# Performance work log

Hardware: AMD Instinct MI355X
Metric: run time of the kernel (lower is better)

The kernel has to match this reference:

```python
import jax, jax.numpy as jnp
from jax import lax
import numpy as np

K = 4            # prototypes per class: 3 kmeans centroids + 1 backbone
EPS = 0.1        # sinkhorn entropic regularization
MAX_ITER = 100
THRESH = 0.01
KM_ITERS = 10    # Lloyd iterations (replaces host-side sklearn KMeans)
HW = 28          # the original reshapes pred to 28x28, fixing n = 784


def setup_inputs():
    key = jax.random.key(0)
    k1, k2, k3, k4 = jax.random.split(key, 4)
    b, n, d, c = 32, HW * HW, 1024, 20
    return {
        "query": jax.random.normal(k1, (b, n, d), dtype=jnp.float32),
        "score": jax.random.uniform(k2, (b, n, c), dtype=jnp.float32),
        "label": jax.random.randint(k3, (b, c), 0, 2),
        "gt": jax.random.randint(k4, (b, HW, HW), 0, c + 1),
        "weights": jnp.array([1.0, 1.0, 0.0, -1.0], dtype=jnp.float32),
    }


def _assign(dq, cen, selfm):
    # dq [b,m,d], cen [b,c,j,d], selfm [b,c,m] float mask -> one-hot labels, counts
    x2 = jnp.sum(dq * dq, axis=-1)                                   # [b,m]
    d2 = (x2[:, None, :, None]
          - 2.0 * jnp.einsum('bmd,bcjd->bcmj', dq, cen)
          + jnp.sum(cen * cen, axis=-1)[:, :, None, :])              # [b,c,m,j]
    oh = jax.nn.one_hot(jnp.argmin(d2, axis=-1), cen.shape[2], dtype=dq.dtype) * selfm[..., None]
    return oh, oh.sum(axis=2)


def _sinkhorn(Km, u, v):
    # vectorized over the [b,c] pair grid, per-pair early exit as in the torch loop
    def cond(st):
        it, r, cc, done = st
        return (it < MAX_ITER) & jnp.logical_not(jnp.all(done))

    def body(st):
        it, r, cc, done = st
        r1 = u / jnp.einsum('bcnj,bcj->bcn', Km, cc)
        c1 = v / jnp.einsum('bcnj,bcn->bcj', Km, r1)
        err = jnp.mean(jnp.abs(r1 - r), axis=-1)                     # [b,c]
        r = jnp.where(done[..., None], r, r1)
        cc = jnp.where(done[..., None], cc, c1)
        done = done | (err < THRESH)
        return it + 1, r, cc, done

    st = (jnp.int32(0), jnp.ones_like(u), jnp.ones_like(v),
          jnp.zeros(Km.shape[:2], dtype=bool))
    _, r, cc, _ = lax.while_loop(cond, body, st)
    return r[..., :, None] * cc[..., None, :] * Km                   # [b,c,n,K]


def _forward(query, score, label, gt, weights):
    b, n, d = query.shape
    c = score.shape[2]
    dq, ds = query[:, ::2, :], score[:, ::2, :]                      # stride-2 downsample
    m = dq.shape[1]
    cls_assign = jnp.argmax(ds, axis=-1)                             # [b,m]
    sel = cls_assign[:, None, :] == jnp.arange(c)[None, :, None]     # [b,c,m]
    selfm = sel.astype(query.dtype)
    cnt = selfm.sum(-1)                                              # [b,c]
    valid = (label > 0) & (cnt >= K)

    # ---- masked Lloyd's k-means with k-1 = 3 clusters per (image, class) pair
    order = jnp.argsort((~sel).astype(jnp.int32), axis=-1)           # masked points first
    init_idx = order[..., :K - 1]                                    # [b,c,3]
    cen = dq[jnp.arange(b)[:, None, None], init_idx]                 # [b,c,3,d]

    def km_step(cen, _):
        oh, kcnt = _assign(dq, cen, selfm)
        sums = jnp.einsum('bmd,bcmj->bcjd', dq, oh)
        cen = jnp.where(kcnt[..., None] > 0,
                        sums / jnp.maximum(kcnt, 1.0)[..., None], cen)
        return cen, None

    cen, _ = lax.scan(km_step, cen, None, length=KM_ITERS)
    oh, kcnt = _assign(dq, cen, selfm)                               # final labels

    # ---- sort centroids by mean cluster score (descending)
    sm = ds.mean(axis=-1)                                            # [b,m]
    avg = jnp.where(kcnt > 0,
                    jnp.einsum('bm,bcmj->bcj', sm, oh) / jnp.maximum(kcnt, 1.0),
                    -jnp.inf)
    ordj = jnp.argsort(-avg, axis=-1)                                # [b,c,3]
    cen = jnp.take_along_axis(cen, ordj[..., None], axis=2)

    # ---- backbone prototype = mean over unselected downsampled tokens
    un = 1.0 - selfm
    backbone = jnp.einsum('bmd,bcm->bcd', dq, un) / jnp.maximum(m - cnt, 1.0)[..., None]
    protos = jnp.concatenate([cen, backbone[:, :, None, :]], axis=2)  # [b,c,4,d]

    # ---- OT between query[0] tokens and the 4 prototypes (original uses query[0] always)
    q0 = query[0]
    q0h = q0 / jnp.maximum(jnp.linalg.norm(q0, axis=-1, keepdims=True), 1e-12)
    ph = protos / jnp.maximum(jnp.linalg.norm(protos, axis=-1, keepdims=True), 1e-12)
    sim = jnp.einsum('nd,bcjd->bcnj', q0h, ph)                       # [b,c,n,4]
    Km = lax.stop_gradient(jnp.exp(-(1.0 - sim) / EPS))              # torch.no_grad
    u = jnp.full((b, c, n), 1.0 / n, dtype=query.dtype)
    v = jnp.full((b, c, K), 1.0 / K, dtype=query.dtype)
    T = lax.stop_gradient(_sinkhorn(Km, u, v))                       # [b,c,n,4]

    valid = valid & jnp.logical_not(jnp.any(jnp.isnan(T), axis=(2, 3)))
    pred = jnp.einsum('bcnj,j->bcn', T, weights)                     # [b,c,n]

    # ---- BCE vs gt masks (28x28 -> 28x28 bilinear resize is the identity)
    y = (gt.reshape(b, -1)[:, None, :] == (jnp.arange(c) + 1)[None, :, None]).astype(pred.dtype)
    p = jnp.clip(pred, 0.0, 1.0)
    bce = -(y * jnp.maximum(jnp.log(p), -100.0)
            + (1.0 - y) * jnp.maximum(jnp.log(1.0 - p), -100.0)).mean(axis=-1)  # [b,c]
    bce = jnp.where(valid, bce, 0.0)
    total_n = valid.sum().astype(pred.dtype)
    return bce.sum() / (total_n + 1e-4)


def reference(query, score, label, gt, weights):
    return _forward(query, score, label, gt, weights)
```

## Files before the change

### kernel.cpp

```cpp
#include <hip/hip_runtime.h>
#include <cmath>

#define BB 32
#define NN 784
#define MM 392
#define DD 1024
#define CC 20
#define JJ 3
#define KP 4
#define KM_ITERS 10
#define GMAX 64
#define SKK 3

__global__ void k_cls(const float* __restrict__ score, int* __restrict__ cls,
                      float* __restrict__ sm, int* __restrict__ cnt) {
  int t = blockIdx.x * blockDim.x + threadIdx.x;
  if (t >= BB * MM) return;
  int b = t / MM, i = t - b * MM;
  const float* s = score + ((size_t)b * NN + 2 * i) * CC;
  float best = s[0]; int bi = 0; float acc = s[0];
  #pragma unroll
  for (int c = 1; c < CC; c++) { float v = s[c]; acc += v; if (v > best) { best = v; bi = c; } }
  cls[t] = bi;
  sm[t] = acc / (float)CC;
  atomicAdd(&cnt[b * CC + bi], 1);
}

__global__ void k_valid(const int* __restrict__ label, const int* __restrict__ cnt,
                        int* __restrict__ vlist, int* __restrict__ cpos, int* __restrict__ nvp) {
  __shared__ int sf[1024];
  int t = threadIdx.x;
  int flag = 0;
  if (t < BB * CC) flag = (label[t] > 0 && cnt[t] >= KP) ? 1 : 0;
  sf[t] = flag;
  __syncthreads();
  for (int off = 1; off < 1024; off <<= 1) {
    int v = sf[t];
    int add = (t >= off) ? sf[t - off] : 0;
    __syncthreads();
    sf[t] = v + add;
    __syncthreads();
  }
  if (t < BB * CC) {
    int pos = sf[t] - flag;
    cpos[t] = flag ? pos : -1;
    if (flag) vlist[pos] = t;
  }
  if (t == 0) *nvp = sf[BB * CC - 1];
}

__global__ __launch_bounds__(512) void k_gram(
    const float* __restrict__ query, const int* __restrict__ cls,
    const int* __restrict__ cpos, const float* __restrict__ sm,
    int* __restrict__ glist, int* __restrict__ gmcnt,
    float* __restrict__ classsum, float* __restrict__ wsort) {
  int bc = blockIdx.x; int b = bc / CC, c = bc - b * CC;
  int tid = threadIdx.x, lane = tid & 63, wv = tid >> 6;
  const float* qb = query + (size_t)b * NN * DD;
  __shared__ int s_scan[512];
  __shared__ int s_list[GMAX];
  __shared__ __align__(16) float Xs[GMAX][68];
  __shared__ float Gl[GMAX][65];
  __shared__ float s_w[JJ][GMAX];

  int flag = 0;
  if (tid < MM) flag = (cls[b * MM + tid] == c) ? 1 : 0;
  s_scan[tid] = flag;
  __syncthreads();
  for (int off = 1; off < 512; off <<= 1) {
    int v = s_scan[tid];
    int add = (tid >= off) ? s_scan[tid - off] : 0;
    __syncthreads();
    s_scan[tid] = v + add;
    __syncthreads();
  }
  if (tid < MM && flag) { int pp = s_scan[tid] - 1; if (pp < GMAX) s_list[pp] = tid; }
  __syncthreads();
  int mc = s_scan[MM - 1]; if (mc > GMAX) mc = GMAX;
  if (tid < mc) glist[bc * GMAX + tid] = s_list[tid];
  if (tid == 0) gmcnt[bc] = mc;
  bool valid = (cpos[bc] >= 0);

  int npairs = mc * (mc + 1) / 2;
  int pi[5], pj[5];
  float pacc[5];
  #pragma unroll
  for (int s = 0; s < 5; s++) {
    pacc[s] = 0.f; pi[s] = -1; pj[s] = 0;
    int p = tid + s * 512;
    if (valid && p < npairs) {
      int i = (int)floorf((sqrtf(8.0f * (float)p + 1.0f) - 1.0f) * 0.5f);
      while ((i + 1) * (i + 2) / 2 <= p) i++;
      while (i * (i + 1) / 2 > p) i--;
      pi[s] = i; pj[s] = p - i * (i + 1) / 2;
    }
  }

  for (int ch = 0; ch < DD / 64; ch++) {
    __syncthreads();
    for (int e = tid; e < mc * 16; e += 512) {
      int row = e >> 4, c4 = e & 15;
      float4 v = *(const float4*)(qb + (size_t)(2 * s_list[row]) * DD + ch * 64 + c4 * 4);
      *(float4*)&Xs[row][c4 * 4] = v;
    }
    __syncthreads();
    #pragma unroll
    for (int s = 0; s < 5; s++) {
      if (pi[s] >= 0) {
        const float4* xi = (const float4*)&Xs[pi[s]][0];
        const float4* xj = (const float4*)&Xs[pj[s]][0];
        float a = 0.f;
        #pragma unroll
        for (int kk = 0; kk < 16; kk++) {
          float4 u = xi[kk], w = xj[kk];
          a += u.x * w.x + u.y * w.y + u.z * w.z + u.w * w.w;
        }
        pacc[s] += a;
      }
    }
    if (tid < 64) {
      float s = 0.f;
      for (int row = 0; row < mc; row++) s += Xs[row][tid];
      classsum[(size_t)bc * DD + ch * 64 + tid] = s;
    }
  }
  if (!valid) return;
  #pragma unroll
  for (int s = 0; s < 5; s++)
    if (pi[s] >= 0) { Gl[pi[s]][pj[s]] = pacc[s]; Gl[pj[s]][pi[s]] = pacc[s]; }
  __syncthreads();

  bool act = lane < mc;
  float smv = act ? sm[b * MM + s_list[lane]] : 0.f;
  if (wv == 0) {
    s_w[0][lane] = (lane == 0) ? 1.f : 0.f;
    s_w[1][lane] = (lane == 1) ? 1.f : 0.f;
    s_w[2][lane] = (lane == 2) ? 1.f : 0.f;
  }
  __syncthreads();
  int aj = 0, n0 = 0, n1 = 0, n2 = 0;
  for (int it = 0; it <= KM_ITERS; it++) {
    float h0 = 0.f, h1 = 0.f, h2 = 0.f;
    if (act) {
      for (int i = 0; i < mc; i++) {
        float g = Gl[lane][i];
        h0 += s_w[0][i] * g; h1 += s_w[1][i] * g; h2 += s_w[2][i] * g;
      }
    }
    float t0 = s_w[0][lane] * h0, t1 = s_w[1][lane] * h1, t2 = s_w[2][lane] * h2;
    for (int o = 1; o < 64; o <<= 1) {
      t0 += __shfl_xor(t0, o, 64); t1 += __shfl_xor(t1, o, 64); t2 += __shfl_xor(t2, o, 64);
    }
    float e0 = t0 - 2.f * h0, e1 = t1 - 2.f * h1, e2 = t2 - 2.f * h2;
    aj = 0; float bv = e0;
    if (e1 < bv) { bv = e1; aj = 1; }
    if (e2 < bv) { bv = e2; aj = 2; }
    n0 = __popcll(__ballot(act && aj == 0));
    n1 = __popcll(__ballot(act && aj == 1));
    n2 = __popcll(__ballot(act && aj == 2));
    if (it == KM_ITERS) break;
    __syncthreads();
    if (act) {
      if (n0 > 0) s_w[0][lane] = (aj == 0) ? 1.f / (float)n0 : 0.f;
      if (n1 > 0) s_w[1][lane] = (aj == 1) ? 1.f / (float)n1 : 0.f;
      if (n2 > 0) s_w[2][lane] = (aj == 2) ? 1.f / (float)n2 : 0.f;
    }
    __syncthreads();
  }
  float s0 = (act && aj == 0) ? smv : 0.f;
  float s1 = (act && aj == 1) ? smv : 0.f;
  float s2 = (act && aj == 2) ? smv : 0.f;
  for (int o = 1; o < 64; o <<= 1) {
    s0 += __shfl_xor(s0, o, 64); s1 += __shfl_xor(s1, o, 64); s2 += __shfl_xor(s2, o, 64);
  }
  if (wv == 0) {
    float avg[JJ];
    avg[0] = (n0 > 0) ? s0 / (float)n0 : -INFINITY;
    avg[1] = (n1 > 0) ? s1 / (float)n1 : -INFINITY;
    avg[2] = (n2 > 0) ? s2 / (float)n2 : -INFINITY;
    int ordv[JJ]; bool used[JJ] = {false, false, false};
    for (int s = 0; s < JJ; s++) {
      int bi = -1; float bv = 0.f;
      for (int j = 0; j < JJ; j++)
        if (!used[j] && (bi < 0 || avg[j] > bv)) { bi = j; bv = avg[j]; }
      used[bi] = true; ordv[s] = bi;
    }
    float* wp = wsort + (size_t)cpos[bc] * (JJ * GMAX);
    wp[0 * GMAX + lane] = s_w[ordv[0]][lane];
    wp[1 * GMAX + lane] = s_w[ordv[1]][lane];
    wp[2 * GMAX + lane] = s_w[ordv[2]][lane];
  }
}

__global__ void k_totalsum(const float* __restrict__ classsum, float* __restrict__ totalsum) {
  int t = blockIdx.x * 256 + threadIdx.x;
  int b = t >> 10, k = t & (DD - 1);
  float s = 0.f;
  for (int c = 0; c < CC; c++) s += classsum[((size_t)b * CC + c) * DD + k];
  totalsum[t] = s;
}

__global__ __launch_bounds__(256) void k_cen(
    const float* __restrict__ query, const int* __restrict__ cpos,
    const int* __restrict__ gmcnt, const int* __restrict__ glist,
    const float* __restrict__ wsort, const float* __restrict__ totalsum,
    const float* __restrict__ classsum, const int* __restrict__ cnt,
    float* __restrict__ ph) {
  int bc = blockIdx.x; int p = cpos[bc];
  if (p < 0) return;
  int b = bc / CC;
  int tid = threadIdx.x, lane = tid & 63, wv = tid >> 6;
  __shared__ float s_wl[JJ][GMAX];
  __shared__ int s_gl[GMAX];
  __shared__ float s_red[4][4];
  __shared__ float s_nrm[4];
  int mc = gmcnt[bc];
  if (tid < JJ * GMAX) s_wl[tid >> 6][tid & 63] = wsort[(size_t)p * (JJ * GMAX) + tid];
  if (tid < GMAX) s_gl[tid] = (tid < mc) ? glist[bc * GMAX + tid] : 0;
  __syncthreads();
  const float* qb = query + (size_t)b * NN * DD;
  float4 a0 = make_float4(0.f, 0.f, 0.f, 0.f), a1 = a0, a2 = a0;
  for (int g = 0; g < mc; g++) {
    float4 v = *(const float4*)(qb + (size_t)(2 * s_gl[g]) * DD + tid * 4);
    float w0 = s_wl[0][g], w1 = s_wl[1][g], w2 = s_wl[2][g];
    a0.x += w0 * v.x; a0.y += w0 * v.y; a0.z += w0 * v.z; a0.w += w0 * v.w;
    a1.x += w1 * v.x; a1.y += w1 * v.y; a1.z += w1 * v.z; a1.w += w1 * v.w;
    a2.x += w2 * v.x; a2.y += w2 * v.y; a2.z += w2 * v.z; a2.w += w2 * v.w;
  }
  float denom = fmaxf((float)(MM - cnt[bc]), 1.f);
  float4 tv = *(const float4*)(totalsum + (size_t)b * DD + tid * 4);
  float4 cv = *(const float4*)(classsum + (size_t)bc * DD + tid * 4);
  float4 a3 = make_float4((tv.x - cv.x) / denom, (tv.y - cv.y) / denom,
                          (tv.z - cv.z) / denom, (tv.w - cv.w) / denom);
  float pp0 = a0.x * a0.x + a0.y * a0.y + a0.z * a0.z + a0.w * a0.w;
  float pp1 = a1.x * a1.x + a1.y * a1.y + a1.z * a1.z + a1.w * a1.w;
  float pp2 = a2.x * a2.x + a2.y * a2.y + a2.z * a2.z + a2.w * a2.w;
  float pp3 = a3.x * a3.x + a3.y * a3.y + a3.z * a3.z + a3.w * a3.w;
  for (int o = 1; o < 64; o <<= 1) {
    pp0 += __shfl_xor(pp0, o, 64); pp1 += __shfl_xor(pp1, o, 64);
    pp2 += __shfl_xor(pp2, o, 64); pp3 += __shfl_xor(pp3, o, 64);
  }
  if (lane == 0) { s_red[wv][0] = pp0; s_red[wv][1] = pp1; s_red[wv][2] = pp2; s_red[wv][3] = pp3; }
  __syncthreads();
  if (tid < 4)
    s_nrm[tid] = fmaxf(sqrtf(s_red[0][tid] + s_red[1][tid] + s_red[2][tid] + s_red[3][tid]), 1e-12f);
  __syncthreads();
  float n0 = s_nrm[0], n1 = s_nrm[1], n2 = s_nrm[2], n3 = s_nrm[3];
  *(float4*)(ph + ((size_t)bc * KP + 0) * DD + tid * 4) =
      make_float4(a0.x / n0, a0.y / n0, a0.z / n0, a0.w / n0);
  *(float4*)(ph + ((size_t)bc * KP + 1) * DD + tid * 4) =
      make_float4(a1.x / n1, a1.y / n1, a1.z / n1, a1.w / n1);
  *(float4*)(ph + ((size_t)bc * KP + 2) * DD + tid * 4) =
      make_float4(a2.x / n2, a2.y / n2, a2.z / n2, a2.w / n2);
  *(float4*)(ph + ((size_t)bc * KP + 3) * DD + tid * 4) =
      make_float4(a3.x / n3, a3.y / n3, a3.z / n3, a3.w / n3);
}

__global__ void k_q0h(const float* __restrict__ query, float* __restrict__ q0h) {
  int n = blockIdx.x;
  const float* src = query + (size_t)n * DD;
  float ss = 0.f;
  for (int k = threadIdx.x; k < DD; k += 64) { float v = src[k]; ss += v * v; }
  for (int o = 32; o > 0; o >>= 1) ss += __shfl_xor(ss, o, 64);
  float nrm = fmaxf(sqrtf(ss), 1e-12f);
  for (int k = threadIdx.x; k < DD; k += 64) q0h[(size_t)n * DD + k] = src[k] / nrm;
}

__global__ __launch_bounds__(256) void k_gemm(const float* __restrict__ A,
    const float* __restrict__ ph, const int* __restrict__ vlist,
    const int* __restrict__ nvp, float* __restrict__ P) {
  int nv4 = 4 * *nvp;
  int n0 = blockIdx.y * 64;
  if (n0 >= nv4) return;
  __shared__ float As[64][20];
  __shared__ float Bs[64][20];
  int tx = threadIdx.x & 15, ty = threadIdx.x >> 4;
  int m0 = blockIdx.x * 64;
  int s = blockIdx.z;
  int lrow = threadIdx.x >> 2;
  int lk = (threadIdx.x & 3) * 4;
  int brow = n0 + lrow;
  bool bval = brow < nv4;
  const float* Brow = ph;
  if (bval) {
    int bcc = brow >> 2;
    Brow = ph + ((size_t)vlist[bcc] * KP + (brow & 3)) * DD;
  }
  float acc[4][4] = {};
  int kbase = s * 352;
  int kend = (kbase + 352 < DD) ? (kbase + 352) : DD;
  for (int k0 = kbase; k0 < kend; k0 += 16) {
    int ar = m0 + lrow;
    float4 av = (ar < NN) ? *(const float4*)(A + (size_t)ar * DD + k0 + lk)
                          : make_float4(0.f, 0.f, 0.f, 0.f);
    *(float4*)&As[lrow][lk] = av;
    float4 bv = bval ? *(const float4*)(Brow + k0 + lk)
                     : make_float4(0.f, 0.f, 0.f, 0.f);
    *(float4*)&Bs[lrow][lk] = bv;
    __syncthreads();
    #pragma unroll
    for (int kk = 0; kk < 16; kk += 4) {
      float4 a4[4], b4[4];
      #pragma unroll
      for (int i = 0; i < 4; i++) a4[i] = *(const float4*)&As[ty * 4 + i][kk];
      #pragma unroll
      for (int j = 0; j < 4; j++) b4[j] = *(const float4*)&Bs[tx + 16 * j][kk];
      #pragma unroll
      for (int i = 0; i < 4; i++)
        #pragma unroll
        for (int j = 0; j < 4; j++) {
          acc[i][j] += a4[i].x * b4[j].x;
          acc[i][j] += a4[i].y * b4[j].y;
          acc[i][j] += a4[i].z * b4[j].z;
          acc[i][j] += a4[i].w * b4[j].w;
        }
    }
    __syncthreads();
  }
  #pragma unroll
  for (int i = 0; i < 4; i++) {
    int mr = m0 + ty * 4 + i;
    if (mr >= NN) continue;
    float* row = P + ((size_t)s * NN + mr) * (size_t)(BB * CC * KP) + n0 + tx;
    #pragma unroll
    for (int j = 0; j < 4; j++) row[16 * j] = acc[i][j];
  }
}

__global__ __launch_bounds__(256) void k_sink(const float* __restrict__ P,
    const int* __restrict__ label, const int* __restrict__ cnt,
    const int* __restrict__ cpos,
    const int* __restrict__ gt, const float* __restrict__ wts,
    float* __restrict__ bce, int* __restrict__ vld) {
  int bc = blockIdx.x; int b = bc / CC, c = bc - b * CC;
  if (label[bc] <= 0 || cnt[bc] < KP) {
    if (threadIdx.x == 0) { bce[bc] = 0.f; vld[bc] = 0; }
    return;
  }
  __shared__ __align__(16) float4 Ks[NN];
  __shared__ float r[NN];
  __shared__ float ccv[KP];
  __shared__ float wred[4][5];
  __shared__ float s_err;
  __shared__ int s_nan;
  int p = cpos[bc];
  const float4* P4 = (const float4*)P;
  for (int t = threadIdx.x; t < NN; t += 256) {
    float4 a = P4[(size_t)(0 * NN + t) * (BB * CC) + p];
    float4 bb = P4[(size_t)(1 * NN + t) * (BB * CC) + p];
    float4 cc3 = P4[(size_t)(2 * NN + t) * (BB * CC) + p];
    float4 o;
    o.x = expf(-(1.0f - (a.x + bb.x + cc3.x)) / 0.1f);
    o.y = expf(-(1.0f - (a.y + bb.y + cc3.y)) / 0.1f);
    o.z = expf(-(1.0f - (a.z + bb.z + cc3.z)) / 0.1f);
    o.w = expf(-(1.0f - (a.w + bb.w + cc3.w)) / 0.1f);
    Ks[t] = o; r[t] = 1.f;
  }
  if (threadIdx.x < KP) ccv[threadIdx.x] = 1.f;
  if (threadIdx.x == 0) s_nan = 0;
  __syncthreads();
  const float uu = 1.0f / (float)NN, vv = 1.0f / (float)KP;
  int lane = threadIdx.x & 63, wv = threadIdx.x >> 6;
  for (int it = 0; it < 100; it++) {
    float c0 = ccv[0], c1 = ccv[1], c2 = ccv[2], c3 = ccv[3];
    float dsum = 0.f, p0 = 0.f, p1 = 0.f, p2 = 0.f, p3 = 0.f;
    for (int n = threadIdx.x; n < NN; n += 256) {
      float4 kv = Ks[n];
      float S = kv.x * c0 + kv.y * c1 + kv.z * c2 + kv.w * c3;
      float r1 = uu / S;
      dsum += fabsf(r1 - r[n]);
      r[n] = r1;
      p0 += kv.x * r1; p1 += kv.y * r1; p2 += kv.z * r1; p3 += kv.w * r1;
    }
    for (int o = 32; o > 0; o >>= 1) {
      dsum += __shfl_down(dsum, o, 64);
      p0 += __shfl_down(p0, o, 64); p1 += __shfl_down(p1, o, 64);
      p2 += __shfl_down(p2, o, 64); p3 += __shfl_down(p3, o, 64);
    }
    if (lane == 0) { wred[wv][0] = dsum; wred[wv][1] = p0; wred[wv][2] = p1; wred[wv][3] = p2; wred[wv][4] = p3; }
    __syncthreads();
    if (threadIdx.x == 0) {
      float d = 0.f, q0 = 0.f, q1 = 0.f, q2 = 0.f, q3 = 0.f;
      for (int w = 0; w < 4; w++) { d += wred[w][0]; q0 += wred[w][1]; q1 += wred[w][2]; q2 += wred[w][3]; q3 += wred[w][4]; }
      ccv[0] = vv / q0; ccv[1] = vv / q1; ccv[2] = vv / q2; ccv[3] = vv / q3;
      s_err = d / (float)NN;
    }
    __syncthreads();
    if (s_err < 0.01f) break;
  }
  float w0 = wts[0], w1 = wts[1], w2 = wts[2], w3 = wts[3];
  float cc0 = ccv[0], cc1 = ccv[1], cc2 = ccv[2], cc3 = ccv[3];
  float bsum = 0.f; int nanloc = 0;
  const int* gtb = gt + b * NN;
  for (int n = threadIdx.x; n < NN; n += 256) {
    float4 kv = Ks[n];
    float rv = r[n];
    float T0 = rv * cc0 * kv.x, T1 = rv * cc1 * kv.y, T2 = rv * cc2 * kv.z, T3 = rv * cc3 * kv.w;
    if (T0 != T0 || T1 != T1 || T2 != T2 || T3 != T3) nanloc = 1;
    float pred = T0 * w0 + T1 * w1 + T2 * w2 + T3 * w3;
    float pcl = fminf(fmaxf(pred, 0.f), 1.f);
    float t = (gtb[n] == c + 1) ? fmaxf(logf(pcl), -100.f) : fmaxf(logf(1.f - pcl), -100.f);
    bsum += t;
  }
  if (nanloc) s_nan = 1;
  for (int o = 32; o > 0; o >>= 1) bsum += __shfl_down(bsum, o, 64);
  if (lane == 0) wred[wv][0] = bsum;
  __syncthreads();
  if (threadIdx.x == 0) {
    float tot = wred[0][0] + wred[1][0] + wred[2][0] + wred[3][0];
    if (s_nan) { bce[bc] = 0.f; vld[bc] = 0; }
    else { bce[bc] = -(tot / (float)NN); vld[bc] = 1; }
  }
}

__global__ void k_final(const float* __restrict__ bce, const int* __restrict__ vld,
                        float* __restrict__ out) {
  __shared__ float rs[256];
  __shared__ float rc[256];
  float s = 0.f, cv = 0.f;
  for (int t = threadIdx.x; t < BB * CC; t += 256) { s += bce[t]; cv += (float)vld[t]; }
  rs[threadIdx.x] = s; rc[threadIdx.x] = cv; __syncthreads();
  for (int o = 128; o > 0; o >>= 1) {
    if (threadIdx.x < o) { rs[threadIdx.x] += rs[threadIdx.x + o]; rc[threadIdx.x] += rc[threadIdx.x + o]; }
    __syncthreads();
  }
  if (threadIdx.x == 0) out[0] = rs[0] / (rc[0] + 0.0001f);
}

extern "C" void kernel_launch(void* const* d_in, const int* in_sizes, int n_in,
                              void* d_out, int out_size, void* d_ws, size_t ws_size,
                              hipStream_t stream) {
  (void)in_sizes; (void)n_in; (void)out_size; (void)ws_size;
  const float* query = (const float*)d_in[0];
  const float* score = (const float*)d_in[1];
  const int*   label = (const int*)d_in[2];
  const int*   gt    = (const int*)d_in[3];
  const float* wts   = (const float*)d_in[4];
  float* ws = (float*)d_ws;

  size_t off = 0;
  int* cls = (int*)(ws + off);       off += (size_t)BB * MM;
  int* cnt = (int*)(ws + off);       off += (size_t)BB * CC;
  float* sm = ws + off;              off += (size_t)BB * MM;
  int* vlist = (int*)(ws + off);     off += (size_t)BB * CC;
  int* cpos = (int*)(ws + off);      off += (size_t)BB * CC;
  int* nvp = (int*)(ws + off);       off += 16;
  int* glist = (int*)(ws + off);     off += (size_t)BB * CC * GMAX;
  int* gmcnt = (int*)(ws + off);     off += (size_t)BB * CC;
  float* wsort = ws + off;           off += (size_t)BB * CC * JJ * GMAX;
  float* classsum = ws + off;        off += (size_t)BB * CC * DD;
  float* totalsum = ws + off;        off += (size_t)BB * DD;
  float* ph = ws + off;              off += (size_t)BB * CC * KP * DD;
  float* q0h = ws + off;             off += (size_t)NN * DD;
  float* P = ws + off;               off += (size_t)SKK * NN * BB * CC * KP;
  float* bce = ws + off;             off += (size_t)BB * CC;
  int* vld = (int*)(ws + off);       off += (size_t)BB * CC;

  hipMemsetAsync(cnt, 0, (size_t)BB * CC * sizeof(int), stream);
  k_cls<<<(BB * MM + 255) / 256, 256, 0, stream>>>(score, cls, sm, cnt);
  k_valid<<<1, 1024, 0, stream>>>(label, cnt, vlist, cpos, nvp);
  k_gram<<<BB * CC, 512, 0, stream>>>(query, cls, cpos, sm, glist, gmcnt, classsum, wsort);
  k_totalsum<<<(BB * DD) / 256, 256, 0, stream>>>(classsum, totalsum);
  k_cen<<<BB * CC, 256, 0, stream>>>(query, cpos, gmcnt, glist, wsort, totalsum,
                                     classsum, cnt, ph);
  k_q0h<<<NN, 64, 0, stream>>>(query, q0h);
  dim3 gg((NN + 63) / 64, (BB * CC * KP) / 64, SKK);
  k_gemm<<<gg, 256, 0, stream>>>(q0h, ph, vlist, nvp, P);
  k_sink<<<BB * CC, 256, 0, stream>>>(P, label, cnt, cpos, gt, wts, bce, vld);
  k_final<<<1, 256, 0, stream>>>(bce, vld, (float*)d_out);
}
```

Baseline: 296.3 us.

## Fuse centroid computation into gram kernel, prefetch loads, keep sinkhorn state in registers

```diff
diff --git a/kernel.cpp b/kernel.cpp
--- a/kernel.cpp
+++ b/kernel.cpp
@@ -52,8 +52,7 @@
 __global__ __launch_bounds__(512) void k_gram(
     const float* __restrict__ query, const int* __restrict__ cls,
     const int* __restrict__ cpos, const float* __restrict__ sm,
-    int* __restrict__ glist, int* __restrict__ gmcnt,
-    float* __restrict__ classsum, float* __restrict__ wsort) {
+    float* __restrict__ classsum, float* __restrict__ ph) {
   int bc = blockIdx.x; int b = bc / CC, c = bc - b * CC;
   int tid = threadIdx.x, lane = tid & 63, wv = tid >> 6;
   const float* qb = query + (size_t)b * NN * DD;
@@ -62,6 +61,7 @@
   __shared__ __align__(16) float Xs[GMAX][68];
   __shared__ float Gl[GMAX][65];
   __shared__ float s_w[JJ][GMAX];
+  __shared__ int s_rank[JJ];
 
   int flag = 0;
   if (tid < MM) flag = (cls[b * MM + tid] == c) ? 1 : 0;
@@ -77,9 +77,22 @@
   if (tid < MM && flag) { int pp = s_scan[tid] - 1; if (pp < GMAX) s_list[pp] = tid; }
   __syncthreads();
   int mc = s_scan[MM - 1]; if (mc > GMAX) mc = GMAX;
-  if (tid < mc) glist[bc * GMAX + tid] = s_list[tid];
-  if (tid == 0) gmcnt[bc] = mc;
   bool valid = (cpos[bc] >= 0);
+
+  const float* pbase0 = nullptr; const float* pbase1 = nullptr;
+  float* xdst0 = nullptr; float* xdst1 = nullptr;
+  {
+    int e0 = tid;
+    if (e0 < mc * 16) {
+      pbase0 = qb + (size_t)(2 * s_list[e0 >> 4]) * DD + (e0 & 15) * 4;
+      xdst0 = &Xs[e0 >> 4][(e0 & 15) * 4];
+    }
+    int e1 = tid + 512;
+    if (e1 < mc * 16) {
+      pbase1 = qb + (size_t)(2 * s_list[e1 >> 4]) * DD + (e1 & 15) * 4;
+      xdst1 = &Xs[e1 >> 4][(e1 & 15) * 4];
+    }
+  }
 
   int npairs = mc * (mc + 1) / 2;
   int pi[5], pj[5];
@@ -96,12 +109,16 @@
     }
   }
 
-  for (int ch = 0; ch < DD / 64; ch++) {
-    __syncthreads();
-    for (int e = tid; e < mc * 16; e += 512) {
-      int row = e >> 4, c4 = e & 15;
-      float4 v = *(const float4*)(qb + (size_t)(2 * s_list[row]) * DD + ch * 64 + c4 * 4);
-      *(float4*)&Xs[row][c4 * 4] = v;
+  float4 cur0, cur1, nxt0, nxt1;
+  if (pbase0) cur0 = *(const float4*)(pbase0);
+  if (pbase1) cur1 = *(const float4*)(pbase1);
+  for (int ch = 0; ch < 16; ch++) {
+    __syncthreads();
+    if (pbase0) *(float4*)xdst0 = cur0;
+    if (pbase1) *(float4*)xdst1 = cur1;
+    if (ch < 15) {
+      if (pbase0) nxt0 = *(const float4*)(pbase0 + (ch + 1) * 64);
+      if (pbase1) nxt1 = *(const float4*)(pbase1 + (ch + 1) * 64);
     }
     __syncthreads();
     #pragma unroll
@@ -118,142 +135,135 @@
         pacc[s] += a;
       }
     }
-    if (tid < 64) {
-      float s = 0.f;
-      for (int row = 0; row < mc; row++) s += Xs[row][tid];
-      classsum[(size_t)bc * DD + ch * 64 + tid] = s;
-    }
+    if (tid >= 448) {
+      int col = tid - 448;
+      float ssum = 0.f;
+      for (int row = 0; row < mc; row++) ssum += Xs[row][col];
+      classsum[(size_t)bc * DD + ch * 64 + col] = ssum;
+    }
+    cur0 = nxt0; cur1 = nxt1;
   }
   if (!valid) return;
+
   #pragma unroll
   for (int s = 0; s < 5; s++)
     if (pi[s] >= 0) { Gl[pi[s]][pj[s]] = pacc[s]; Gl[pj[s]][pi[s]] = pacc[s]; }
   __syncthreads();
 
-  bool act = lane < mc;
-  float smv = act ? sm[b * MM + s_list[lane]] : 0.f;
   if (wv == 0) {
+    bool act = lane < mc;
+    float smv = act ? sm[b * MM + s_list[lane]] : 0.f;
     s_w[0][lane] = (lane == 0) ? 1.f : 0.f;
     s_w[1][lane] = (lane == 1) ? 1.f : 0.f;
     s_w[2][lane] = (lane == 2) ? 1.f : 0.f;
-  }
-  __syncthreads();
-  int aj = 0, n0 = 0, n1 = 0, n2 = 0;
-  for (int it = 0; it <= KM_ITERS; it++) {
-    float h0 = 0.f, h1 = 0.f, h2 = 0.f;
-    if (act) {
-      for (int i = 0; i < mc; i++) {
-        float g = Gl[lane][i];
-        h0 += s_w[0][i] * g; h1 += s_w[1][i] * g; h2 += s_w[2][i] * g;
-      }
-    }
-    float t0 = s_w[0][lane] * h0, t1 = s_w[1][lane] * h1, t2 = s_w[2][lane] * h2;
+    int aj = 0, n0 = 0, n1 = 0, n2 = 0;
+    for (int it = 0; it <= KM_ITERS; it++) {
+      float h0 = 0.f, h1 = 0.f, h2 = 0.f;
+      if (act) {
+        for (int i = 0; i < mc; i++) {
+          float g = Gl[lane][i];
+          h0 += s_w[0][i] * g; h1 += s_w[1][i] * g; h2 += s_w[2][i] * g;
+        }
+      }
+      float t0 = s_w[0][lane] * h0, t1 = s_w[1][lane] * h1, t2 = s_w[2][lane] * h2;
+      for (int o = 1; o < 64; o <<= 1) {
+        t0 += __shfl_xor(t0, o, 64); t1 += __shfl_xor(t1, o, 64); t2 += __shfl_xor(t2, o, 64);
+      }
+      float e0 = t0 - 2.f * h0, e1 = t1 - 2.f * h1, e2 = t2 - 2.f * h2;
+      aj = 0; float bv = e0;
+      if (e1 < bv) { bv = e1; aj = 1; }
+      if (e2 < bv) { bv = e2; aj = 2; }
+      n0 = __popcll(__ballot(act && aj == 0));
+      n1 = __popcll(__ballot(act && aj == 1));
+      n2 = __popcll(__ballot(act && aj == 2));
+      if (it == KM_ITERS) break;
+      if (act) {
+        if (n0 > 0) s_w[0][lane] = (aj == 0) ? 1.f / (float)n0 : 0.f;
+        if (n1 > 0) s_w[1][lane] = (aj == 1) ? 1.f / (float)n1 : 0.f;
+        if (n2 > 0) s_w[2][lane] = (aj == 2) ? 1.f / (float)n2 : 0.f;
+      }
+    }
+    float s0 = (act && aj == 0) ? smv : 0.f;
+    float s1 = (act && aj == 1) ? smv : 0.f;
+    float s2 = (act && aj == 2) ? smv : 0.f;
     for (int o = 1; o < 64; o <<= 1) {
-      t0 += __shfl_xor(t0, o, 64); t1 += __shfl_xor(t1, o, 64); t2 += __shfl_xor(t2, o, 64);
-    }
-    float e0 = t0 - 2.f * h0, e1 = t1 - 2.f * h1, e2 = t2 - 2.f * h2;
-    aj = 0; float bv = e0;
-    if (e1 < bv) { bv = e1; aj = 1; }
-    if (e2 < bv) { bv = e2; aj = 2; }
-    n0 = __popcll(__ballot(act && aj == 0));
-    n1 = __popcll(__ballot(act && aj == 1));
-    n2 = __popcll(__ballot(act && aj == 2));
-    if (it == KM_ITERS) break;
-    __syncthreads();
-    if (act) {
-      if (n0 > 0) s_w[0][lane] = (aj == 0) ? 1.f / (float)n0 : 0.f;
-      if (n1 > 0) s_w[1][lane] = (aj == 1) ? 1.f / (float)n1 : 0.f;
-      if (n2 > 0) s_w[2][lane] = (aj == 2) ? 1.f / (float)n2 : 0.f;
-    }
-    __syncthreads();
-  }
-  float s0 = (act && aj == 0) ? smv : 0.f;
-  float s1 = (act && aj == 1) ? smv : 0.f;
-  float s2 = (act && aj == 2) ? smv : 0.f;
-  for (int o = 1; o < 64; o <<= 1) {
-    s0 += __shfl_xor(s0, o, 64); s1 += __shfl_xor(s1, o, 64); s2 += __shfl_xor(s2, o, 64);
-  }
-  if (wv == 0) {
-    float avg[JJ];
-    avg[0] = (n0 > 0) ? s0 / (float)n0 : -INFINITY;
-    avg[1] = (n1 > 0) ? s1 / (float)n1 : -INFINITY;
-    avg[2] = (n2 > 0) ? s2 / (float)n2 : -INFINITY;
-    int ordv[JJ]; bool used[JJ] = {false, false, false};
-    for (int s = 0; s < JJ; s++) {
-      int bi = -1; float bv = 0.f;
-      for (int j = 0; j < JJ; j++)
-        if (!used[j] && (bi < 0 || avg[j] > bv)) { bi = j; bv = avg[j]; }
-      used[bi] = true; ordv[s] = bi;
-    }
-    float* wp = wsort + (size_t)cpos[bc] * (JJ * GMAX);
-    wp[0 * GMAX + lane] = s_w[ordv[0]][lane];
-    wp[1 * GMAX + lane] = s_w[ordv[1]][lane];
-    wp[2 * GMAX + lane] = s_w[ordv[2]][lane];
-  }
-}
-
-__global__ void k_totalsum(const float* __restrict__ classsum, float* __restrict__ totalsum) {
-  int t = blockIdx.x * 256 + threadIdx.x;
-  int b = t >> 10, k = t & (DD - 1);
-  float s = 0.f;
-  for (int c = 0; c < CC; c++) s += classsum[((size_t)b * CC + c) * DD + k];
-  totalsum[t] = s;
-}
-
-__global__ __launch_bounds__(256) void k_cen(
-    const float* __restrict__ query, const int* __restrict__ cpos,
-    const int* __restrict__ gmcnt, const int* __restrict__ glist,
-    const float* __restrict__ wsort, const float* __restrict__ totalsum,
-    const float* __restrict__ classsum, const int* __restrict__ cnt,
-    float* __restrict__ ph) {
-  int bc = blockIdx.x; int p = cpos[bc];
-  if (p < 0) return;
+      s0 += __shfl_xor(s0, o, 64); s1 += __shfl_xor(s1, o, 64); s2 += __shfl_xor(s2, o, 64);
+    }
+    if (lane == 0) {
+      float avg[JJ];
+      avg[0] = (n0 > 0) ? s0 / (float)n0 : -INFINITY;
+      avg[1] = (n1 > 0) ? s1 / (float)n1 : -INFINITY;
+      avg[2] = (n2 > 0) ? s2 / (float)n2 : -INFINITY;
+      bool used[JJ] = {false, false, false};
+      for (int s = 0; s < JJ; s++) {
+        int bi = -1; float bv = 0.f;
+        for (int j = 0; j < JJ; j++)
+          if (!used[j] && (bi < 0 || avg[j] > bv)) { bi = j; bv = avg[j]; }
+        used[bi] = true; s_rank[bi] = s;
+      }
+    }
+  }
+  __syncthreads();
+
+  float cenv[16];
+  if (pbase0) cur0 = *(const float4*)(pbase0);
+  if (pbase1) cur1 = *(const float4*)(pbase1);
+  for (int ch = 0; ch < 16; ch++) {
+    __syncthreads();
+    if (pbase0) *(float4*)xdst0 = cur0;
+    if (pbase1) *(float4*)xdst1 = cur1;
+    if (ch < 15) {
+      if (pbase0) nxt0 = *(const float4*)(pbase0 + (ch + 1) * 64);
+      if (pbase1) nxt1 = *(const float4*)(pbase1 + (ch + 1) * 64);
+    }
+    __syncthreads();
+    if (tid < 192) {
+      int j = tid >> 6, l = tid & 63;
+      float a = 0.f;
+      for (int g = 0; g < mc; g++) a += s_w[j][g] * Xs[g][l];
+      cenv[ch] = a;
+    }
+    cur0 = nxt0; cur1 = nxt1;
+  }
+  if (tid < 192) {
+    int j = tid >> 6, l = tid & 63;
+    float ssq = 0.f;
+    #pragma unroll
+    for (int ch = 0; ch < 16; ch++) ssq += cenv[ch] * cenv[ch];
+    for (int o = 1; o < 64; o <<= 1) ssq += __shfl_xor(ssq, o, 64);
+    float nrm = fmaxf(sqrtf(ssq), 1e-12f);
+    float* dst = ph + ((size_t)bc * KP + s_rank[j]) * DD + l;
+    #pragma unroll
+    for (int ch = 0; ch < 16; ch++) dst[ch * 64] = cenv[ch] / nrm;
+  }
+}
+
+__global__ __launch_bounds__(256) void k_backbone(const float* __restrict__ classsum,
+    const int* __restrict__ cpos, const int* __restrict__ cnt, float* __restrict__ ph) {
+  int bc = blockIdx.x;
+  if (cpos[bc] < 0) return;
   int b = bc / CC;
   int tid = threadIdx.x, lane = tid & 63, wv = tid >> 6;
-  __shared__ float s_wl[JJ][GMAX];
-  __shared__ int s_gl[GMAX];
-  __shared__ float s_red[4][4];
-  __shared__ float s_nrm[4];
-  int mc = gmcnt[bc];
-  if (tid < JJ * GMAX) s_wl[tid >> 6][tid & 63] = wsort[(size_t)p * (JJ * GMAX) + tid];
-  if (tid < GMAX) s_gl[tid] = (tid < mc) ? glist[bc * GMAX + tid] : 0;
-  __syncthreads();
-  const float* qb = query + (size_t)b * NN * DD;
-  float4 a0 = make_float4(0.f, 0.f, 0.f, 0.f), a1 = a0, a2 = a0;
-  for (int g = 0; g < mc; g++) {
-    float4 v = *(const float4*)(qb + (size_t)(2 * s_gl[g]) * DD + tid * 4);
-    float w0 = s_wl[0][g], w1 = s_wl[1][g], w2 = s_wl[2][g];
-    a0.x += w0 * v.x; a0.y += w0 * v.y; a0.z += w0 * v.z; a0.w += w0 * v.w;
-    a1.x += w1 * v.x; a1.y += w1 * v.y; a1.z += w1 * v.z; a1.w += w1 * v.w;
-    a2.x += w2 * v.x; a2.y += w2 * v.y; a2.z += w2 * v.z; a2.w += w2 * v.w;
-  }
+  __shared__ float s_red[4];
+  __shared__ float s_nrm;
+  float4 ts = make_float4(0.f, 0.f, 0.f, 0.f);
+  for (int c2 = 0; c2 < CC; c2++) {
+    float4 v = *(const float4*)(classsum + ((size_t)(b * CC + c2)) * DD + tid * 4);
+    ts.x += v.x; ts.y += v.y; ts.z += v.z; ts.w += v.w;
+  }
+  float4 cs = *(const float4*)(classsum + (size_t)bc * DD + tid * 4);
   float denom = fmaxf((float)(MM - cnt[bc]), 1.f);
-  float4 tv = *(const float4*)(totalsum + (size_t)b * DD + tid * 4);
-  float4 cv = *(const float4*)(classsum + (size_t)bc * DD + tid * 4);
-  float4 a3 = make_float4((tv.x - cv.x) / denom, (tv.y - cv.y) / denom,
-                          (tv.z - cv.z) / denom, (tv.w - cv.w) / denom);
-  float pp0 = a0.x * a0.x + a0.y * a0.y + a0.z * a0.z + a0.w * a0.w;
-  float pp1 = a1.x * a1.x + a1.y * a1.y + a1.z * a1.z + a1.w * a1.w;
-  float pp2 = a2.x * a2.x + a2.y * a2.y + a2.z * a2.z + a2.w * a2.w;
-  float pp3 = a3.x * a3.x + a3.y * a3.y + a3.z * a3.z + a3.w * a3.w;
-  for (int o = 1; o < 64; o <<= 1) {
-    pp0 += __shfl_xor(pp0, o, 64); pp1 += __shfl_xor(pp1, o, 64);
-    pp2 += __shfl_xor(pp2, o, 64); pp3 += __shfl_xor(pp3, o, 64);
-  }
-  if (lane == 0) { s_red[wv][0] = pp0; s_red[wv][1] = pp1; s_red[wv][2] = pp2; s_red[wv][3] = pp3; }
-  __syncthreads();
-  if (tid < 4)
-    s_nrm[tid] = fmaxf(sqrtf(s_red[0][tid] + s_red[1][tid] + s_red[2][tid] + s_red[3][tid]), 1e-12f);
-  __syncthreads();
-  float n0 = s_nrm[0], n1 = s_nrm[1], n2 = s_nrm[2], n3 = s_nrm[3];
-  *(float4*)(ph + ((size_t)bc * KP + 0) * DD + tid * 4) =
-      make_float4(a0.x / n0, a0.y / n0, a0.z / n0, a0.w / n0);
-  *(float4*)(ph + ((size_t)bc * KP + 1) * DD + tid * 4) =
-      make_float4(a1.x / n1, a1.y / n1, a1.z / n1, a1.w / n1);
-  *(float4*)(ph + ((size_t)bc * KP + 2) * DD + tid * 4) =
-      make_float4(a2.x / n2, a2.y / n2, a2.z / n2, a2.w / n2);
+  float4 v = make_float4((ts.x - cs.x) / denom, (ts.y - cs.y) / denom,
+                         (ts.z - cs.z) / denom, (ts.w - cs.w) / denom);
+  float pp = v.x * v.x + v.y * v.y + v.z * v.z + v.w * v.w;
+  for (int o = 1; o < 64; o <<= 1) pp += __shfl_xor(pp, o, 64);
+  if (lane == 0) s_red[wv] = pp;
+  __syncthreads();
+  if (tid == 0) s_nrm = fmaxf(sqrtf(s_red[0] + s_red[1] + s_red[2] + s_red[3]), 1e-12f);
+  __syncthreads();
+  float nrm = s_nrm;
   *(float4*)(ph + ((size_t)bc * KP + 3) * DD + tid * 4) =
-      make_float4(a3.x / n3, a3.y / n3, a3.z / n3, a3.w / n3);
+      make_float4(v.x / nrm, v.y / nrm, v.z / nrm, v.w / nrm);
 }
 
 __global__ void k_q0h(const float* __restrict__ query, float* __restrict__ q0h) {
@@ -328,49 +338,56 @@
 }
 
 __global__ __launch_bounds__(256) void k_sink(const float* __restrict__ P,
-    const int* __restrict__ label, const int* __restrict__ cnt,
-    const int* __restrict__ cpos,
-    const int* __restrict__ gt, const float* __restrict__ wts,
-    float* __restrict__ bce, int* __restrict__ vld) {
+    const int* __restrict__ cpos, const int* __restrict__ gt,
+    const float* __restrict__ wts, float* __restrict__ bce, int* __restrict__ vld) {
   int bc = blockIdx.x; int b = bc / CC, c = bc - b * CC;
-  if (label[bc] <= 0 || cnt[bc] < KP) {
-    if (threadIdx.x == 0) { bce[bc] = 0.f; vld[bc] = 0; }
+  int tid = threadIdx.x;
+  if (cpos[bc] < 0) {
+    if (tid == 0) { bce[bc] = 0.f; vld[bc] = 0; }
     return;
   }
-  __shared__ __align__(16) float4 Ks[NN];
-  __shared__ float r[NN];
+  int p = cpos[bc];
+  int lane = tid & 63, wv = tid >> 6;
   __shared__ float ccv[KP];
   __shared__ float wred[4][5];
   __shared__ float s_err;
   __shared__ int s_nan;
-  int p = cpos[bc];
   const float4* P4 = (const float4*)P;
-  for (int t = threadIdx.x; t < NN; t += 256) {
-    float4 a = P4[(size_t)(0 * NN + t) * (BB * CC) + p];
-    float4 bb = P4[(size_t)(1 * NN + t) * (BB * CC) + p];
-    float4 cc3 = P4[(size_t)(2 * NN + t) * (BB * CC) + p];
-    float4 o;
-    o.x = expf(-(1.0f - (a.x + bb.x + cc3.x)) / 0.1f);
-    o.y = expf(-(1.0f - (a.y + bb.y + cc3.y)) / 0.1f);
-    o.z = expf(-(1.0f - (a.z + bb.z + cc3.z)) / 0.1f);
-    o.w = expf(-(1.0f - (a.w + bb.w + cc3.w)) / 0.1f);
-    Ks[t] = o; r[t] = 1.f;
-  }
-  if (threadIdx.x < KP) ccv[threadIdx.x] = 1.f;
-  if (threadIdx.x == 0) s_nan = 0;
+  float4 kv[4]; float rr[4];
+  #pragma unroll
+  for (int s = 0; s < 4; s++) {
+    int n = tid + 256 * s;
+    kv[s] = make_float4(0.f, 0.f, 0.f, 0.f); rr[s] = 1.f;
+    if (n < NN) {
+      float4 a = P4[(size_t)(0 * NN + n) * (BB * CC) + p];
+      float4 b2 = P4[(size_t)(1 * NN + n) * (BB * CC) + p];
+      float4 c2 = P4[(size_t)(2 * NN + n) * (BB * CC) + p];
+      float4 o;
+      o.x = expf(-(1.0f - (a.x + b2.x + c2.x)) / 0.1f);
+      o.y = expf(-(1.0f - (a.y + b2.y + c2.y)) / 0.1f);
+      o.z = expf(-(1.0f - (a.z + b2.z + c2.z)) / 0.1f);
+      o.w = expf(-(1.0f - (a.w + b2.w + c2.w)) / 0.1f);
+      kv[s] = o;
+    }
+  }
+  if (tid < KP) ccv[tid] = 1.f;
+  if (tid == 0) s_nan = 0;
   __syncthreads();
   const float uu = 1.0f / (float)NN, vv = 1.0f / (float)KP;
-  int lane = threadIdx.x & 63, wv = threadIdx.x >> 6;
   for (int it = 0; it < 100; it++) {
     float c0 = ccv[0], c1 = ccv[1], c2 = ccv[2], c3 = ccv[3];
     float dsum = 0.f, p0 = 0.f, p1 = 0.f, p2 = 0.f, p3 = 0.f;
-    for (int n = threadIdx.x; n < NN; n += 256) {
-      float4 kv = Ks[n];
-      float S = kv.x * c0 + kv.y * c1 + kv.z * c2 + kv.w * c3;
-      float r1 = uu / S;
-      dsum += fabsf(r1 - r[n]);
-      r[n] = r1;
-      p0 += kv.x * r1; p1 += kv.y * r1; p2 += kv.z * r1; p3 += kv.w * r1;
+    #pragma unroll
+    for (int s = 0; s < 4; s++) {
+      int n = tid + 256 * s;
+      if (n < NN) {
+        float4 k4 = kv[s];
+        float S = k4.x * c0 + k4.y * c1 + k4.z * c2 + k4.w * c3;
+        float r1 = uu / S;
+        dsum += fabsf(r1 - rr[s]);
+        rr[s] = r1;
+        p0 += k4.x * r1; p1 += k4.y * r1; p2 += k4.z * r1; p3 += k4.w * r1;
+      }
     }
     for (int o = 32; o > 0; o >>= 1) {
       dsum += __shfl_down(dsum, o, 64);
@@ -379,7 +396,7 @@
     }
     if (lane == 0) { wred[wv][0] = dsum; wred[wv][1] = p0; wred[wv][2] = p1; wred[wv][3] = p2; wred[wv][4] = p3; }
     __syncthreads();
-    if (threadIdx.x == 0) {
+    if (tid == 0) {
       float d = 0.f, q0 = 0.f, q1 = 0.f, q2 = 0.f, q3 = 0.f;
       for (int w = 0; w < 4; w++) { d += wred[w][0]; q0 += wred[w][1]; q1 += wred[w][2]; q2 += wred[w][3]; q3 += wred[w][4]; }
       ccv[0] = vv / q0; ccv[1] = vv / q1; ccv[2] = vv / q2; ccv[3] = vv / q3;
@@ -392,21 +409,25 @@
   float cc0 = ccv[0], cc1 = ccv[1], cc2 = ccv[2], cc3 = ccv[3];
   float bsum = 0.f; int nanloc = 0;
   const int* gtb = gt + b * NN;
-  for (int n = threadIdx.x; n < NN; n += 256) {
-    float4 kv = Ks[n];
-    float rv = r[n];
-    float T0 = rv * cc0 * kv.x, T1 = rv * cc1 * kv.y, T2 = rv * cc2 * kv.z, T3 = rv * cc3 * kv.w;
-    if (T0 != T0 || T1 != T1 || T2 != T2 || T3 != T3) nanloc = 1;
-    float pred = T0 * w0 + T1 * w1 + T2 * w2 + T3 * w3;
-    float pcl = fminf(fmaxf(pred, 0.f), 1.f);
-    float t = (gtb[n] == c + 1) ? fmaxf(logf(pcl), -100.f) : fmaxf(logf(1.f - pcl), -100.f);
-    bsum += t;
+  #pragma unroll
+  for (int s = 0; s < 4; s++) {
+    int n = tid + 256 * s;
+    if (n < NN) {
+      float4 k4 = kv[s];
+      float rv = rr[s];
+      float T0 = rv * cc0 * k4.x, T1 = rv * cc1 * k4.y, T2 = rv * cc2 * k4.z, T3 = rv * cc3 * k4.w;
+      if (T0 != T0 || T1 != T1 || T2 != T2 || T3 != T3) nanloc = 1;
+      float pred = T0 * w0 + T1 * w1 + T2 * w2 + T3 * w3;
+      float pcl = fminf(fmaxf(pred, 0.f), 1.f);
+      float t = (gtb[n] == c + 1) ? fmaxf(logf(pcl), -100.f) : fmaxf(logf(1.f - pcl), -100.f);
+      bsum += t;
+    }
   }
   if (nanloc) s_nan = 1;
   for (int o = 32; o > 0; o >>= 1) bsum += __shfl_down(bsum, o, 64);
   if (lane == 0) wred[wv][0] = bsum;
   __syncthreads();
-  if (threadIdx.x == 0) {
+  if (tid == 0) {
     float tot = wred[0][0] + wred[1][0] + wred[2][0] + wred[3][0];
     if (s_nan) { bce[bc] = 0.f; vld[bc] = 0; }
     else { bce[bc] = -(tot / (float)NN); vld[bc] = 1; }
@@ -445,11 +466,7 @@
   int* vlist = (int*)(ws + off);     off += (size_t)BB * CC;
   int* cpos = (int*)(ws + off);      off += (size_t)BB * CC;
   int* nvp = (int*)(ws + off);       off += 16;
-  int* glist = (int*)(ws + off);     off += (size_t)BB * CC * GMAX;
-  int* gmcnt = (int*)(ws + off);     off += (size_t)BB * CC;
-  float* wsort = ws + off;           off += (size_t)BB * CC * JJ * GMAX;
   float* classsum = ws + off;        off += (size_t)BB * CC * DD;
-  float* totalsum = ws + off;        off += (size_t)BB * DD;
   float* ph = ws + off;              off += (size_t)BB * CC * KP * DD;
   float* q0h = ws + off;             off += (size_t)NN * DD;
   float* P = ws + off;               off += (size_t)SKK * NN * BB * CC * KP;
@@ -459,13 +476,11 @@
   hipMemsetAsync(cnt, 0, (size_t)BB * CC * sizeof(int), stream);
   k_cls<<<(BB * MM + 255) / 256, 256, 0, stream>>>(score, cls, sm, cnt);
   k_valid<<<1, 1024, 0, stream>>>(label, cnt, vlist, cpos, nvp);
-  k_gram<<<BB * CC, 512, 0, stream>>>(query, cls, cpos, sm, glist, gmcnt, classsum, wsort);
-  k_totalsum<<<(BB * DD) / 256, 256, 0, stream>>>(classsum, totalsum);
-  k_cen<<<BB * CC, 256, 0, stream>>>(query, cpos, gmcnt, glist, wsort, totalsum,
-                                     classsum, cnt, ph);
+  k_gram<<<BB * CC, 512, 0, stream>>>(query, cls, cpos, sm, classsum, ph);
+  k_backbone<<<BB * CC, 256, 0, stream>>>(classsum, cpos, cnt, ph);
   k_q0h<<<NN, 64, 0, stream>>>(query, q0h);
   dim3 gg((NN + 63) / 64, (BB * CC * KP) / 64, SKK);
   k_gemm<<<gg, 256, 0, stream>>>(q0h, ph, vlist, nvp, P);
-  k_sink<<<BB * CC, 256, 0, stream>>>(P, label, cnt, cpos, gt, wts, bce, vld);
+  k_sink<<<BB * CC, 256, 0, stream>>>(P, cpos, gt, wts, bce, vld);
   k_final<<<1, 256, 0, stream>>>(bce, vld, (float*)d_out);
 }
```

New measurement: 294.4 us. No clear change (-0.6%).
